# Kernel tuning notes

Measured on AMD Instinct MI355X. Metric: run time of the kernel, lower is better.

Reference implementation:

```python
import jax, jax.numpy as jnp
import numpy as np

B = 32          # batch size
N_IN = 1000000  # dofs of source function space (CG1 mesh)
N_OUT = 500000  # number of evaluation points (DG0 on VertexOnlyMesh)
K = 3           # nonzeros per row (CG1 barycentric interpolation)


def setup_inputs() -> dict:
    key = jax.random.key(0)
    k1, k2, k3 = jax.random.split(key, 3)
    x = jax.random.normal(k1, (B, N_IN), dtype=jnp.float32)
    # barycentric-style weights: nonnegative, rows sum to 1
    w_raw = jax.random.uniform(k2, (N_OUT, K), dtype=jnp.float32)
    w = w_raw / jnp.sum(w_raw, axis=1, keepdims=True)
    idx = jax.random.randint(k3, (N_OUT, K), 0, N_IN, dtype=jnp.int32)
    return {"x": x, "w": w, "idx": idx}


def reference(x, w, idx):
    # y = A @ x^T per sample, with A the sparse interpolation operator:
    # y[b, o] = sum_k w[o, k] * x[b, idx[o, k]]
    gathered = x[:, idx]                      # [B, N_OUT, K] gather
    return jnp.einsum("ok,bok->bo", w, gathered)  # [B, N_OUT]
```

## Files before the change

### kernel.cpp

```cpp
#include <hip/hip_runtime.h>
#include <hip/hip_bf16.h>

#define B_DIM 32
#define N_IN 1000000
#define N_OUT 500000

typedef float nfloat4 __attribute__((ext_vector_type(4)));

__device__ __forceinline__ unsigned int f32_to_bf16_rne(float f) {
    unsigned int u = __float_as_uint(f);
    unsigned int rounding = 0x7fffu + ((u >> 16) & 1u);
    return (u + rounding) >> 16;
}

__global__ __launch_bounds__(256) void transpose_bf16_kernel(
    const float* __restrict__ x, unsigned short* __restrict__ xT)
{
    __shared__ unsigned int tile[64][17];
    const int t  = threadIdx.x;
    const int i0 = blockIdx.x * 64;

    const int qi = t & 15;
    const int p  = t >> 4;

    const float* r0 = x + (size_t)(2 * p)     * N_IN + i0 + qi * 4;
    const float* r1 = x + (size_t)(2 * p + 1) * N_IN + i0 + qi * 4;
    const nfloat4 va = __builtin_nontemporal_load((const nfloat4*)r0);
    const nfloat4 vb = __builtin_nontemporal_load((const nfloat4*)r1);

    tile[qi * 4 + 0][p] = f32_to_bf16_rne(va.x) | (f32_to_bf16_rne(vb.x) << 16);
    tile[qi * 4 + 1][p] = f32_to_bf16_rne(va.y) | (f32_to_bf16_rne(vb.y) << 16);
    tile[qi * 4 + 2][p] = f32_to_bf16_rne(va.z) | (f32_to_bf16_rne(vb.z) << 16);
    tile[qi * 4 + 3][p] = f32_to_bf16_rne(va.w) | (f32_to_bf16_rne(vb.w) << 16);
    __syncthreads();

    const int ii = t >> 2;
    const int g  = t & 3;
    uint4 pk;
    pk.x = tile[ii][g * 4 + 0];
    pk.y = tile[ii][g * 4 + 1];
    pk.z = tile[ii][g * 4 + 2];
    pk.w = tile[ii][g * 4 + 3];
    *(uint4*)((char*)xT + (size_t)(i0 + ii) * 64 + g * 16) = pk;
}

__global__ __launch_bounds__(256, 6) void gather_bf16_v3_kernel(
    const unsigned short* __restrict__ xT,
    const float* __restrict__ w,
    const int*   __restrict__ idx,
    float* __restrict__ out)
{
    const int t = threadIdx.x;
    const int g = t >> 2;
    const int l = t & 3;
    const int base0 = blockIdx.x * 128;
    const int oa = base0 + g;
    const int ob = base0 + 64 + g;
    if (oa >= N_OUT) return;
    const bool has_b = (ob < N_OUT);

    const int ba = 3 * oa;
    const int   ia0 = __builtin_nontemporal_load(idx + ba + 0);
    const int   ia1 = __builtin_nontemporal_load(idx + ba + 1);
    const int   ia2 = __builtin_nontemporal_load(idx + ba + 2);
    const float wa0 = __builtin_nontemporal_load(w + ba + 0);
    const float wa1 = __builtin_nontemporal_load(w + ba + 1);
    const float wa2 = __builtin_nontemporal_load(w + ba + 2);

    int   ib0 = 0, ib1 = 0, ib2 = 0;
    float wb0 = 0.f, wb1 = 0.f, wb2 = 0.f;
    if (has_b) {
        const int bb = 3 * ob;
        ib0 = __builtin_nontemporal_load(idx + bb + 0);
        ib1 = __builtin_nontemporal_load(idx + bb + 1);
        ib2 = __builtin_nontemporal_load(idx + bb + 2);
        wb0 = __builtin_nontemporal_load(w + bb + 0);
        wb1 = __builtin_nontemporal_load(w + bb + 1);
        wb2 = __builtin_nontemporal_load(w + bb + 2);
    }

    const uint4 va0 = *(const uint4*)(xT + (size_t)ia0 * B_DIM + l * 8);
    const uint4 va1 = *(const uint4*)(xT + (size_t)ia1 * B_DIM + l * 8);
    const uint4 va2 = *(const uint4*)(xT + (size_t)ia2 * B_DIM + l * 8);
    const uint4 vb0 = *(const uint4*)(xT + (size_t)ib0 * B_DIM + l * 8);
    const uint4 vb1 = *(const uint4*)(xT + (size_t)ib1 * B_DIM + l * 8);
    const uint4 vb2 = *(const uint4*)(xT + (size_t)ib2 * B_DIM + l * 8);

    float acca[8], accb[8];
#pragma unroll
    for (int j = 0; j < 8; ++j) { acca[j] = 0.0f; accb[j] = 0.0f; }

    const unsigned int ua0[4] = {va0.x, va0.y, va0.z, va0.w};
    const unsigned int ua1[4] = {va1.x, va1.y, va1.z, va1.w};
    const unsigned int ua2[4] = {va2.x, va2.y, va2.z, va2.w};
    const unsigned int ub0[4] = {vb0.x, vb0.y, vb0.z, vb0.w};
    const unsigned int ub1[4] = {vb1.x, vb1.y, vb1.z, vb1.w};
    const unsigned int ub2[4] = {vb2.x, vb2.y, vb2.z, vb2.w};
#pragma unroll
    for (int m = 0; m < 4; ++m) {
        float a = acca[2 * m], c = acca[2 * m + 1];
        a = fmaf(wa0, __uint_as_float(ua0[m] << 16), a);
        c = fmaf(wa0, __uint_as_float(ua0[m] & 0xffff0000u), c);
        a = fmaf(wa1, __uint_as_float(ua1[m] << 16), a);
        c = fmaf(wa1, __uint_as_float(ua1[m] & 0xffff0000u), c);
        a = fmaf(wa2, __uint_as_float(ua2[m] << 16), a);
        c = fmaf(wa2, __uint_as_float(ua2[m] & 0xffff0000u), c);
        acca[2 * m] = a; acca[2 * m + 1] = c;

        float d = accb[2 * m], e = accb[2 * m + 1];
        d = fmaf(wb0, __uint_as_float(ub0[m] << 16), d);
        e = fmaf(wb0, __uint_as_float(ub0[m] & 0xffff0000u), e);
        d = fmaf(wb1, __uint_as_float(ub1[m] << 16), d);
        e = fmaf(wb1, __uint_as_float(ub1[m] & 0xffff0000u), e);
        d = fmaf(wb2, __uint_as_float(ub2[m] << 16), d);
        e = fmaf(wb2, __uint_as_float(ub2[m] & 0xffff0000u), e);
        accb[2 * m] = d; accb[2 * m + 1] = e;
    }

    float* obase_a = out + (size_t)(8 * l) * N_OUT + oa;
#pragma unroll
    for (int j = 0; j < 8; ++j) {
        __builtin_nontemporal_store(acca[j], obase_a + (size_t)j * N_OUT);
    }
    if (has_b) {
        float* obase_b = out + (size_t)(8 * l) * N_OUT + ob;
#pragma unroll
        for (int j = 0; j < 8; ++j) {
            __builtin_nontemporal_store(accb[j], obase_b + (size_t)j * N_OUT);
        }
    }
}

__global__ __launch_bounds__(256) void direct_kernel(
    const float* __restrict__ x,
    const float* __restrict__ w,
    const int*   __restrict__ idx,
    float* __restrict__ out)
{
    const int o = blockIdx.x * blockDim.x + threadIdx.x;
    if (o >= N_OUT) return;
    const int base = 3 * o;
    const int i0 = idx[base + 0], i1 = idx[base + 1], i2 = idx[base + 2];
    const float w0 = w[base + 0], w1 = w[base + 1], w2 = w[base + 2];
#pragma unroll 4
    for (int b = 0; b < B_DIM; ++b) {
        const float* __restrict__ xr = x + (size_t)b * N_IN;
        float acc = w0 * xr[i0];
        acc = fmaf(w1, xr[i1], acc);
        acc = fmaf(w2, xr[i2], acc);
        out[(size_t)b * N_OUT + o] = acc;
    }
}

extern "C" void kernel_launch(void* const* d_in, const int* in_sizes, int n_in,
                              void* d_out, int out_size, void* d_ws, size_t ws_size,
                              hipStream_t stream) {
    const float* x   = (const float*)d_in[0];
    const float* w   = (const float*)d_in[1];
    const int*   idx = (const int*)d_in[2];
    float* out = (float*)d_out;

    const size_t xt_bytes = (size_t)N_IN * B_DIM * sizeof(unsigned short);

    if (ws_size >= xt_bytes) {
        unsigned short* xT = (unsigned short*)d_ws;
        transpose_bf16_kernel<<<N_IN / 64, 256, 0, stream>>>(x, xT);
        const int blocks = (N_OUT + 127) / 128;
        gather_bf16_v3_kernel<<<blocks, 256, 0, stream>>>(xT, w, idx, out);
    } else {
        const int blocks = (N_OUT + 255) / 256;
        direct_kernel<<<blocks, 256, 0, stream>>>(x, w, idx, out);
    }
}
```

Measured before the change: 246.5 us.

## Enlarge transpose tile to 256 columns with eight row loads per thread

The fp32-to-bf16 transpose kernel now processes 256 input columns per block instead of 64. Each thread loads eight rows with 16-byte nontemporal loads, packs bf16 pairs, and writes uint4 rows into a padded shared tile. The write-back then loops four times per thread. This gives more memory-level parallelism per thread and a quarter as many blocks, at the cost of more registers, a larger shared tile and possible LDS bank conflicts on the strided column reads.

```diff
diff --git a/kernel.cpp b/kernel.cpp
--- a/kernel.cpp
+++ b/kernel.cpp
@@ -13,35 +13,53 @@
     return (u + rounding) >> 16;
 }
 
-__global__ __launch_bounds__(256) void transpose_bf16_kernel(
+__global__ __launch_bounds__(256) void transpose_bf16_v2_kernel(
     const float* __restrict__ x, unsigned short* __restrict__ xT)
 {
-    __shared__ unsigned int tile[64][17];
+    __shared__ unsigned int tile[16][260];
     const int t  = threadIdx.x;
-    const int i0 = blockIdx.x * 64;
+    const int i0 = blockIdx.x * 256;
 
-    const int qi = t & 15;
-    const int p  = t >> 4;
+    const int qi = t & 63;
+    const int p  = t >> 6;
 
-    const float* r0 = x + (size_t)(2 * p)     * N_IN + i0 + qi * 4;
-    const float* r1 = x + (size_t)(2 * p + 1) * N_IN + i0 + qi * 4;
-    const nfloat4 va = __builtin_nontemporal_load((const nfloat4*)r0);
-    const nfloat4 vb = __builtin_nontemporal_load((const nfloat4*)r1);
+    const bool valid_col = (i0 + 4 * qi) < N_IN;
 
-    tile[qi * 4 + 0][p] = f32_to_bf16_rne(va.x) | (f32_to_bf16_rne(vb.x) << 16);
-    tile[qi * 4 + 1][p] = f32_to_bf16_rne(va.y) | (f32_to_bf16_rne(vb.y) << 16);
-    tile[qi * 4 + 2][p] = f32_to_bf16_rne(va.z) | (f32_to_bf16_rne(vb.z) << 16);
-    tile[qi * 4 + 3][p] = f32_to_bf16_rne(va.w) | (f32_to_bf16_rne(vb.w) << 16);
+    if (valid_col) {
+        const float* rbase = x + (size_t)(8 * p) * N_IN + i0 + 4 * qi;
+        nfloat4 v[8];
+#pragma unroll
+        for (int j = 0; j < 8; ++j) {
+            v[j] = __builtin_nontemporal_load(
+                (const nfloat4*)(rbase + (size_t)j * N_IN));
+        }
+#pragma unroll
+        for (int m = 0; m < 4; ++m) {
+            uint4 pk;
+            pk.x = f32_to_bf16_rne(v[2*m].x) | (f32_to_bf16_rne(v[2*m+1].x) << 16);
+            pk.y = f32_to_bf16_rne(v[2*m].y) | (f32_to_bf16_rne(v[2*m+1].y) << 16);
+            pk.z = f32_to_bf16_rne(v[2*m].z) | (f32_to_bf16_rne(v[2*m+1].z) << 16);
+            pk.w = f32_to_bf16_rne(v[2*m].w) | (f32_to_bf16_rne(v[2*m+1].w) << 16);
+            *(uint4*)&tile[4 * p + m][4 * qi] = pk;
+        }
+    }
     __syncthreads();
 
-    const int ii = t >> 2;
-    const int g  = t & 3;
-    uint4 pk;
-    pk.x = tile[ii][g * 4 + 0];
-    pk.y = tile[ii][g * 4 + 1];
-    pk.z = tile[ii][g * 4 + 2];
-    pk.w = tile[ii][g * 4 + 3];
-    *(uint4*)((char*)xT + (size_t)(i0 + ii) * 64 + g * 16) = pk;
+    const int g2 = t & 3;
+    const int i2 = t >> 2;
+#pragma unroll
+    for (int ss = 0; ss < 4; ++ss) {
+        const int col  = ss * 64 + i2;
+        const int irow = i0 + col;
+        if (irow < N_IN) {
+            uint4 pk;
+            pk.x = tile[4 * g2 + 0][col];
+            pk.y = tile[4 * g2 + 1][col];
+            pk.z = tile[4 * g2 + 2][col];
+            pk.w = tile[4 * g2 + 3][col];
+            *(uint4*)((char*)xT + (size_t)irow * 64 + g2 * 16) = pk;
+        }
+    }
 }
 
 __global__ __launch_bounds__(256, 6) void gather_bf16_v3_kernel(
@@ -164,7 +182,8 @@
 
     if (ws_size >= xt_bytes) {
         unsigned short* xT = (unsigned short*)d_ws;
-        transpose_bf16_kernel<<<N_IN / 64, 256, 0, stream>>>(x, xT);
+        const int tblocks = (N_IN + 255) / 256;
+        transpose_bf16_v2_kernel<<<tblocks, 256, 0, stream>>>(x, xT);
         const int blocks = (N_OUT + 127) / 128;
         gather_bf16_v3_kernel<<<blocks, 256, 0, stream>>>(xT, w, idx, out);
     } else {
```

Measured after the change: 250.2 us. No clear change (+1.5%).
